# Kernel optimization log

Hardware: AMD Instinct MI355X
Metric: run time of the kernel (lower is better)

The kernel has to match this reference:

```python
import jax, jax.numpy as jnp
import numpy as np

SEQ_LEN, USER_LEN = 20, 256
INPUT_SIZE = 100000
NUM_CENTROIDS = 64
CAND = 1024
HIDDEN_DIM = 128
TOPK = 10
RHO = 0.02


def setup_inputs() -> dict:
    key = jax.random.key(0)
    ks = jax.random.split(key, 20)
    s = 0.1  # modest weight scale
    return {
        "x": jax.random.randint(ks[0], (SEQ_LEN, USER_LEN), 0, INPUT_SIZE),
        "t_slot": jax.random.randint(ks[1], (SEQ_LEN, USER_LEN), 0, 168),
        "vecs_use": jax.random.normal(ks[2], (INPUT_SIZE, 20), jnp.float32),
        "x_embedding_network": jax.random.normal(ks[3], (INPUT_SIZE, HIDDEN_DIM), jnp.float32),
        "I_array": jax.random.randint(ks[4], (INPUT_SIZE,), 0, NUM_CENTROIDS),
        "cand": jax.random.randint(ks[5], (NUM_CENTROIDS, CAND), 0, INPUT_SIZE),
        "time_embeddings": jax.random.normal(ks[6], (4, 20), jnp.float32),
        "W_seq1": jax.random.normal(ks[7], (100, 40), jnp.float32) * s,
        "b_seq1": jnp.zeros((40,), jnp.float32),
        "W_seq2": jax.random.normal(ks[8], (40, 20), jnp.float32) * s,
        "b_seq2": jnp.zeros((20,), jnp.float32),
        "W_to1": jax.random.normal(ks[9], (40, 40), jnp.float32) * s,
        "b_to1": jnp.zeros((40,), jnp.float32),
        "W_to2": jax.random.normal(ks[10], (40, 20), jnp.float32) * s,
        "b_to2": jnp.zeros((20,), jnp.float32),
        "W_ti1": jax.random.normal(ks[11], (40, 40), jnp.float32) * s,
        "b_ti1": jnp.zeros((40,), jnp.float32),
        "W_ti2": jax.random.normal(ks[12], (40, 20), jnp.float32) * s,
        "b_ti2": jnp.zeros((20,), jnp.float32),
    }


def _map_hour_to_segment(t):
    h = t % 24
    return jnp.where((h >= 22) | (h < 6), 0, jnp.where(h < 14, 1, 2))


def reference(x, t_slot, vecs_use, x_embedding_network, I_array, cand,
              time_embeddings, W_seq1, b_seq1, W_seq2, b_seq2,
              W_to1, b_to1, W_to2, b_to2, W_ti1, b_ti1, W_ti2, b_ti2):
    seq_len, user_len = x.shape
    x_view = x.reshape(-1)                                  # [N]
    x_emb = vecs_use[x_view].reshape(seq_len, user_len, 20)  # [S,U,20]

    # time-transfer (outgoing): concat(loc_emb, time_emb[segment]) -> MLP
    seg = _map_hour_to_segment(t_slot.reshape(-1))
    xc = jnp.concatenate([x_emb.reshape(-1, 20), time_embeddings[seg]], axis=-1)
    xi_out = jax.nn.relu(xc @ W_to1 + b_to1) @ W_to2 + b_to2  # [N,20]

    # candidate side: every location paired with fixed target segment 2
    seg2 = jnp.broadcast_to(time_embeddings[2], (vecs_use.shape[0], 20))
    vo = jnp.concatenate([vecs_use, seg2], axis=-1)
    vec_output = jax.nn.relu(vo @ W_ti1 + b_ti1) @ W_ti2 + b_ti2  # [V,20]

    # 5-step history (shift-with-edge-repeat) concat -> seq MLP
    def shift(k):
        return jnp.concatenate([x_emb[:k], x_emb[:seq_len - k]], axis=0)
    hist = jnp.concatenate(
        [shift(4), shift(3), shift(2), shift(1), x_emb], axis=-1).reshape(-1, 100)
    hist = jax.nn.relu(hist @ W_seq1 + b_seq1) @ W_seq2 + b_seq2  # [N,20]

    # per-token cluster routing + candidate distances
    a = 0.5 * (hist + xi_out)            # [N,20]
    c_idx = I_array[x_view]              # [N] cluster of each token's location
    cand_tok = cand[c_idx]               # [N,C] candidate loc ids
    Vg = vec_output[cand_tok]            # [N,C,20]
    d2 = (jnp.sum(a * a, -1)[:, None] + jnp.sum(Vg * Vg, -1)
          - 2.0 * jnp.einsum('nd,ncd->nc', a, Vg))
    dist = jnp.sqrt(jnp.maximum(d2, 1e-12))
    score = jnp.exp(-RHO * dist)         # [N,C]

    values, idx = jax.lax.top_k(score, TOPK)                 # [N,K]
    neigh_ids = jnp.take_along_axis(cand_tok, idx, axis=1)   # [N,K]
    emb_neigh = x_embedding_network[neigh_ids]               # [N,K,H]
    self_emb = x_embedding_network[x_view][:, None, :]       # [N,1,H]
    emb_all = jnp.concatenate([emb_neigh, self_emb], axis=1)  # [N,K+1,H]
    vals = jnp.concatenate(
        [values, jnp.ones((values.shape[0], 1), values.dtype)], axis=-1)
    w = jax.nn.softmax(vals, axis=-1)                        # [N,K+1]
    return jnp.sum(emb_all * w[..., None], axis=1)           # [N,H]
```

## Files before the change

### kernel.cpp

```cpp
#include <hip/hip_runtime.h>
#include <hip/hip_bf16.h>

#define SEQ_LEN   20
#define USER_LEN  256
#define NTOK      (SEQ_LEN * USER_LEN)
#define NC        64
#define CAND_N    1024
#define HID       128
#define TOPK      10
#define RHO_C     0.02f

#define CAND_BLKS 256
#define TO_BLKS   (NTOK / 256)
#define SEQ_BLKS  (NTOK / 256)
#define MAXB      (NTOK / 8 + NC)

__global__ __launch_bounds__(256) void k_pre(
    const int* __restrict__ x, const int* __restrict__ t_slot,
    const float* __restrict__ vecs, const float* __restrict__ temb,
    const int* __restrict__ I_array, const int* __restrict__ cand,
    const float* __restrict__ Ws1, const float* __restrict__ bs1,
    const float* __restrict__ Ws2, const float* __restrict__ bs2,
    const float* __restrict__ Wt1, const float* __restrict__ bt1,
    const float* __restrict__ Wt2, const float* __restrict__ bt2,
    const float* __restrict__ Wc1, const float* __restrict__ bc1,
    const float* __restrict__ Wc2, const float* __restrict__ bc2,
    float* __restrict__ tab, float* __restrict__ aX, float* __restrict__ aH,
    int* __restrict__ bucket, int* __restrict__ blkInfo) {
  __shared__ float sWS[4800];
  int tid = threadIdx.x;

  if (blockIdx.x < CAND_BLKS) {
    {
      float4* dst = (float4*)sWS;
      const float4* s1 = (const float4*)Wc1;
      for (int i = tid; i < 400; i += 256) dst[i] = s1[i];
      const float4* s2 = (const float4*)Wc2;
      for (int i = tid; i < 200; i += 256) dst[400 + i] = s2[i];
    }
    __syncthreads();
    const float* sW1 = sWS;
    const float* sW2 = sWS + 1600;

    int g = blockIdx.x * 256 + tid;
    int v = cand[g];
    const float4* vp = (const float4*)(vecs + (size_t)v * 20);
    const float4* tp = (const float4*)(temb + 40);

    float o[20];
    #pragma unroll
    for (int k = 0; k < 20; k++) o[k] = bc2[k];

    #pragma unroll 1
    for (int cc = 0; cc < 5; cc++) {
      float hc[8];
      #pragma unroll
      for (int jj = 0; jj < 8; jj++) hc[jj] = bc1[cc * 8 + jj];
      #pragma unroll
      for (int q = 0; q < 5; q++) {
        float4 e = tp[q];
        #pragma unroll
        for (int r = 0; r < 4; r++) {
          float xi = (&e.x)[r];
          const float* wr = &sW1[(20 + 4 * q + r) * 40 + cc * 8];
          float4 w0 = *(const float4*)(wr);
          float4 w1 = *(const float4*)(wr + 4);
          hc[0] = fmaf(xi, w0.x, hc[0]); hc[1] = fmaf(xi, w0.y, hc[1]);
          hc[2] = fmaf(xi, w0.z, hc[2]); hc[3] = fmaf(xi, w0.w, hc[3]);
          hc[4] = fmaf(xi, w1.x, hc[4]); hc[5] = fmaf(xi, w1.y, hc[5]);
          hc[6] = fmaf(xi, w1.z, hc[6]); hc[7] = fmaf(xi, w1.w, hc[7]);
        }
      }
      #pragma unroll
      for (int q = 0; q < 5; q++) {
        float4 e = vp[q];
        #pragma unroll
        for (int r = 0; r < 4; r++) {
          float xi = (&e.x)[r];
          const float* wr = &sW1[(4 * q + r) * 40 + cc * 8];
          float4 w0 = *(const float4*)(wr);
          float4 w1 = *(const float4*)(wr + 4);
          hc[0] = fmaf(xi, w0.x, hc[0]); hc[1] = fmaf(xi, w0.y, hc[1]);
          hc[2] = fmaf(xi, w0.z, hc[2]); hc[3] = fmaf(xi, w0.w, hc[3]);
          hc[4] = fmaf(xi, w1.x, hc[4]); hc[5] = fmaf(xi, w1.y, hc[5]);
          hc[6] = fmaf(xi, w1.z, hc[6]); hc[7] = fmaf(xi, w1.w, hc[7]);
        }
      }
      #pragma unroll
      for (int jj = 0; jj < 8; jj++) {
        float hv = fmaxf(hc[jj], 0.f);
        const float* wr = &sW2[(cc * 8 + jj) * 20];
        #pragma unroll
        for (int kq = 0; kq < 5; kq++) {
          float4 w = *(const float4*)(wr + 4 * kq);
          o[kq * 4 + 0] = fmaf(hv, w.x, o[kq * 4 + 0]);
          o[kq * 4 + 1] = fmaf(hv, w.y, o[kq * 4 + 1]);
          o[kq * 4 + 2] = fmaf(hv, w.z, o[kq * 4 + 2]);
          o[kq * 4 + 3] = fmaf(hv, w.w, o[kq * 4 + 3]);
        }
      }
    }
    int c = g >> 10, j = g & 1023;
    float* op = tab + (size_t)c * (21 * CAND_N) + j;
    float nrm = 0.f;
    #pragma unroll
    for (int k = 0; k < 20; k++) {
      op[k * CAND_N] = o[k];
      nrm = fmaf(o[k], o[k], nrm);
    }
    op[20 * CAND_N] = nrm;

  } else if (blockIdx.x < CAND_BLKS + TO_BLKS) {
    {
      float4* dst = (float4*)sWS;
      const float4* s1 = (const float4*)Wt1;
      for (int i = tid; i < 400; i += 256) dst[i] = s1[i];
      const float4* s2 = (const float4*)Wt2;
      for (int i = tid; i < 200; i += 256) dst[400 + i] = s2[i];
    }
    __syncthreads();
    const float* sW1 = sWS;
    const float* sW2 = sWS + 1600;

    int n = (blockIdx.x - CAND_BLKS) * 256 + tid;
    int xv = x[n];
    int ts = t_slot[n];
    int h24 = ts % 24;
    int seg = (h24 >= 22 || h24 < 6) ? 0 : (h24 < 14 ? 1 : 2);
    const float4* ep = (const float4*)(vecs + (size_t)xv * 20);
    const float4* tp = (const float4*)(temb + seg * 20);

    float o[20];
    #pragma unroll
    for (int k = 0; k < 20; k++) o[k] = bt2[k];

    #pragma unroll 1
    for (int cc = 0; cc < 5; cc++) {
      float hc[8];
      #pragma unroll
      for (int jj = 0; jj < 8; jj++) hc[jj] = bt1[cc * 8 + jj];
      #pragma unroll
      for (int q = 0; q < 5; q++) {
        float4 e = ep[q];
        #pragma unroll
        for (int r = 0; r < 4; r++) {
          float xi = (&e.x)[r];
          const float* wr = &sW1[(4 * q + r) * 40 + cc * 8];
          float4 w0 = *(const float4*)(wr);
          float4 w1 = *(const float4*)(wr + 4);
          hc[0] = fmaf(xi, w0.x, hc[0]); hc[1] = fmaf(xi, w0.y, hc[1]);
          hc[2] = fmaf(xi, w0.z, hc[2]); hc[3] = fmaf(xi, w0.w, hc[3]);
          hc[4] = fmaf(xi, w1.x, hc[4]); hc[5] = fmaf(xi, w1.y, hc[5]);
          hc[6] = fmaf(xi, w1.z, hc[6]); hc[7] = fmaf(xi, w1.w, hc[7]);
        }
      }
      #pragma unroll
      for (int q = 0; q < 5; q++) {
        float4 e = tp[q];
        #pragma unroll
        for (int r = 0; r < 4; r++) {
          float xi = (&e.x)[r];
          const float* wr = &sW1[(20 + 4 * q + r) * 40 + cc * 8];
          float4 w0 = *(const float4*)(wr);
          float4 w1 = *(const float4*)(wr + 4);
          hc[0] = fmaf(xi, w0.x, hc[0]); hc[1] = fmaf(xi, w0.y, hc[1]);
          hc[2] = fmaf(xi, w0.z, hc[2]); hc[3] = fmaf(xi, w0.w, hc[3]);
          hc[4] = fmaf(xi, w1.x, hc[4]); hc[5] = fmaf(xi, w1.y, hc[5]);
          hc[6] = fmaf(xi, w1.z, hc[6]); hc[7] = fmaf(xi, w1.w, hc[7]);
        }
      }
      #pragma unroll
      for (int jj = 0; jj < 8; jj++) {
        float hv = fmaxf(hc[jj], 0.f);
        const float* wr = &sW2[(cc * 8 + jj) * 20];
        #pragma unroll
        for (int kq = 0; kq < 5; kq++) {
          float4 w = *(const float4*)(wr + 4 * kq);
          o[kq * 4 + 0] = fmaf(hv, w.x, o[kq * 4 + 0]);
          o[kq * 4 + 1] = fmaf(hv, w.y, o[kq * 4 + 1]);
          o[kq * 4 + 2] = fmaf(hv, w.z, o[kq * 4 + 2]);
          o[kq * 4 + 3] = fmaf(hv, w.w, o[kq * 4 + 3]);
        }
      }
    }
    #pragma unroll
    for (int k = 0; k < 20; k++) aX[n * 20 + k] = o[k];

  } else if (blockIdx.x < CAND_BLKS + TO_BLKS + SEQ_BLKS) {
    {
      float4* dst = (float4*)sWS;
      const float4* s1 = (const float4*)Ws1;
      for (int i = tid; i < 1000; i += 256) dst[i] = s1[i];
      const float4* s2 = (const float4*)Ws2;
      for (int i = tid; i < 200; i += 256) dst[1000 + i] = s2[i];
    }
    __syncthreads();
    const float* sW1 = sWS;
    const float* sW2 = sWS + 4000;

    int n = (blockIdx.x - CAND_BLKS - TO_BLKS) * 256 + tid;
    int s = n >> 8, u = n & 255;
    int xv2[5];
    #pragma unroll
    for (int b = 0; b < 5; b++) {
      int sh = 4 - b;
      int row = (s >= sh) ? s - sh : s;
      xv2[b] = x[row * USER_LEN + u];
    }

    float o[20];
    #pragma unroll
    for (int k = 0; k < 20; k++) o[k] = bs2[k];

    #pragma unroll 1
    for (int cc = 0; cc < 5; cc++) {
      float hc[8];
      #pragma unroll
      for (int jj = 0; jj < 8; jj++) hc[jj] = bs1[cc * 8 + jj];
      #pragma unroll 1
      for (int b = 0; b < 5; b++) {
        const float4* p = (const float4*)(vecs + (size_t)xv2[b] * 20);
        #pragma unroll
        for (int q = 0; q < 5; q++) {
          float4 e = p[q];
          #pragma unroll
          for (int r = 0; r < 4; r++) {
            float xi = (&e.x)[r];
            const float* wr = &sW1[(b * 20 + 4 * q + r) * 40 + cc * 8];
            float4 w0 = *(const float4*)(wr);
            float4 w1 = *(const float4*)(wr + 4);
            hc[0] = fmaf(xi, w0.x, hc[0]); hc[1] = fmaf(xi, w0.y, hc[1]);
            hc[2] = fmaf(xi, w0.z, hc[2]); hc[3] = fmaf(xi, w0.w, hc[3]);
            hc[4] = fmaf(xi, w1.x, hc[4]); hc[5] = fmaf(xi, w1.y, hc[5]);
            hc[6] = fmaf(xi, w1.z, hc[6]); hc[7] = fmaf(xi, w1.w, hc[7]);
          }
        }
      }
      #pragma unroll
      for (int jj = 0; jj < 8; jj++) {
        float hv = fmaxf(hc[jj], 0.f);
        const float* wr = &sW2[(cc * 8 + jj) * 20];
        #pragma unroll
        for (int kq = 0; kq < 5; kq++) {
          float4 w = *(const float4*)(wr + 4 * kq);
          o[kq * 4 + 0] = fmaf(hv, w.x, o[kq * 4 + 0]);
          o[kq * 4 + 1] = fmaf(hv, w.y, o[kq * 4 + 1]);
          o[kq * 4 + 2] = fmaf(hv, w.z, o[kq * 4 + 2]);
          o[kq * 4 + 3] = fmaf(hv, w.w, o[kq * 4 + 3]);
        }
      }
    }
    #pragma unroll
    for (int k = 0; k < 20; k++) aH[n * 20 + k] = o[k];

  } else {
    int* lc = (int*)sWS;
    int* lcur = lc + NC;
    if (tid < NC) lc[tid] = 0;
    for (int b = tid; b < MAXB; b += 256) blkInfo[b] = -1;
    __syncthreads();
    for (int n = tid; n < NTOK; n += 256)
      atomicAdd(&lc[I_array[x[n]]], 1);
    __syncthreads();

    int v = 0, myStart = 0, nb = 0, blkStart = 0;
    if (tid < 64) {
      v = lc[tid];
      int inc = v;
      #pragma unroll
      for (int d = 1; d < 64; d <<= 1) {
        int t2 = __shfl_up(inc, d);
        if (tid >= d) inc += t2;
      }
      myStart = inc - v;
      lcur[tid] = myStart;
      nb = (v + 7) >> 3;
      int nbs = nb;
      #pragma unroll
      for (int d = 1; d < 64; d <<= 1) {
        int t2 = __shfl_up(nbs, d);
        if (tid >= d) nbs += t2;
      }
      blkStart = nbs - nb;
    }
    __syncthreads();
    for (int n = tid; n < NTOK; n += 256) {
      int c = I_array[x[n]];
      int p = atomicAdd(&lcur[c], 1);
      bucket[p] = n;
    }
    if (tid < 64) {
      for (int k = 0; k < nb; k++) {
        int rem = v - 8 * k;
        int tc = rem < 8 ? rem : 8;
        blkInfo[blkStart + k] = (tid << 20) | (tc << 16) | (myStart + 8 * k);
      }
    }
  }
}

__global__ __launch_bounds__(256) void k_distsel(
    const int* __restrict__ blkInfo, const int* __restrict__ bucket,
    const float* __restrict__ tab, const float* __restrict__ aX,
    const float* __restrict__ aH, const int* __restrict__ x,
    const int* __restrict__ cand, const float* __restrict__ emb,
    float* __restrict__ out) {
  int info = blkInfo[blockIdx.x];
  if (info < 0) return;
  int start = info & 0xFFFF;
  int tcnt  = (info >> 16) & 0xF;
  int c     = info >> 20;

  __shared__ float sA[8][20];
  __shared__ float sN[8];
  __shared__ int   sTok[8];
  __shared__ float sD[8][CAND_N];

  int tid = threadIdx.x;
  if (tid < 8) sTok[tid] = (tid < tcnt) ? bucket[start + tid] : -1;
  if (tid < 160) {
    int tt = tid / 20, d = tid - tt * 20;
    if (tt < tcnt) {
      int n = bucket[start + tt];
      sA[tt][d] = 0.5f * (aH[n * 20 + d] + aX[n * 20 + d]);
    } else {
      sA[tt][d] = 0.f;
    }
  }
  __syncthreads();
  if (tid < 8) {
    float nrm = 0.f;
    #pragma unroll
    for (int d = 0; d < 20; d++) nrm = fmaf(sA[tid][d], sA[tid][d], nrm);
    sN[tid] = nrm;
  }
  __syncthreads();

  const float* T = tab + (size_t)c * (21 * CAND_N);
  int j4 = tid * 4;
  float4 acc[8];
  #pragma unroll
  for (int tt = 0; tt < 8; tt++) acc[tt] = make_float4(0.f, 0.f, 0.f, 0.f);
  #pragma unroll
  for (int dq = 0; dq < 5; dq++) {
    float4 t0 = *(const float4*)(T + (dq * 4 + 0) * CAND_N + j4);
    float4 t1 = *(const float4*)(T + (dq * 4 + 1) * CAND_N + j4);
    float4 t2 = *(const float4*)(T + (dq * 4 + 2) * CAND_N + j4);
    float4 t3 = *(const float4*)(T + (dq * 4 + 3) * CAND_N + j4);
    #pragma unroll
    for (int tt = 0; tt < 8; tt++) {
      float4 av = *(const float4*)(&sA[tt][dq * 4]);
      acc[tt].x = fmaf(av.x, t0.x, acc[tt].x);
      acc[tt].y = fmaf(av.x, t0.y, acc[tt].y);
      acc[tt].z = fmaf(av.x, t0.z, acc[tt].z);
      acc[tt].w = fmaf(av.x, t0.w, acc[tt].w);
      acc[tt].x = fmaf(av.y, t1.x, acc[tt].x);
      acc[tt].y = fmaf(av.y, t1.y, acc[tt].y);
      acc[tt].z = fmaf(av.y, t1.z, acc[tt].z);
      acc[tt].w = fmaf(av.y, t1.w, acc[tt].w);
      acc[tt].x = fmaf(av.z, t2.x, acc[tt].x);
      acc[tt].y = fmaf(av.z, t2.y, acc[tt].y);
      acc[tt].z = fmaf(av.z, t2.z, acc[tt].z);
      acc[tt].w = fmaf(av.z, t2.w, acc[tt].w);
      acc[tt].x = fmaf(av.w, t3.x, acc[tt].x);
      acc[tt].y = fmaf(av.w, t3.y, acc[tt].y);
      acc[tt].z = fmaf(av.w, t3.z, acc[tt].z);
      acc[tt].w = fmaf(av.w, t3.w, acc[tt].w);
    }
  }
  float4 cn4 = *(const float4*)(T + 20 * CAND_N + j4);
  #pragma unroll
  for (int tt = 0; tt < 8; tt++) {
    float4 d2;
    d2.x = sN[tt] + cn4.x - 2.f * acc[tt].x;
    d2.y = sN[tt] + cn4.y - 2.f * acc[tt].y;
    d2.z = sN[tt] + cn4.z - 2.f * acc[tt].z;
    d2.w = sN[tt] + cn4.w - 2.f * acc[tt].w;
    *(float4*)(&sD[tt][j4]) = d2;
  }
  __syncthreads();

  int lane = tid & 63, w = tid >> 6;
  #pragma unroll 1
  for (int pass = 0; pass < 2; pass++) {
    int tt = w + 4 * pass;
    if (tt >= tcnt) continue;
    int n = sTok[tt];
    int xv = x[n];

    float v[16];
    #pragma unroll
    for (int m = 0; m < 16; m++) v[m] = sD[tt][m * 64 + lane];

    float acc0 = 0.f, acc1 = 0.f, esum = 0.f;
    #pragma unroll 1
    for (int r = 0; r < TOPK; r++) {
      float bv = v[0];
      int bj = lane;
      #pragma unroll
      for (int m = 1; m < 16; m++) {
        int jm = (m << 6) | lane;
        if (v[m] < bv) { bv = v[m]; bj = jm; }
      }
      #pragma unroll
      for (int o = 1; o < 64; o <<= 1) {
        float ov = __shfl_xor(bv, o);
        int   oj = __shfl_xor(bj, o);
        if (ov < bv || (ov == bv && oj < bj)) { bv = ov; bj = oj; }
      }
      float dist = sqrtf(fmaxf(bv, 1e-12f));
      float e = expf(expf(-RHO_C * dist));
      int id = cand[c * CAND_N + bj];
      esum += e;
      acc0 = fmaf(e, emb[(size_t)id * HID + lane], acc0);
      acc1 = fmaf(e, emb[(size_t)id * HID + 64 + lane], acc1);
      #pragma unroll
      for (int m = 0; m < 16; m++) {
        int jm = (m << 6) | lane;
        if (jm == bj) v[m] = 3.0e38f;
      }
    }
    const float e1 = 2.71828182845904523536f;
    esum += e1;
    acc0 = fmaf(e1, emb[(size_t)xv * HID + lane], acc0);
    acc1 = fmaf(e1, emb[(size_t)xv * HID + 64 + lane], acc1);
    float inv = 1.0f / esum;
    out[(size_t)n * HID + lane] = acc0 * inv;
    out[(size_t)n * HID + 64 + lane] = acc1 * inv;
  }
}

extern "C" void kernel_launch(void* const* d_in, const int* in_sizes, int n_in,
                              void* d_out, int out_size, void* d_ws, size_t ws_size,
                              hipStream_t stream) {
  const int*   x      = (const int*)d_in[0];
  const int*   t_slot = (const int*)d_in[1];
  const float* vecs   = (const float*)d_in[2];
  const float* embn   = (const float*)d_in[3];
  const int*   I_arr  = (const int*)d_in[4];
  const int*   cand   = (const int*)d_in[5];
  const float* temb   = (const float*)d_in[6];
  const float* Ws1    = (const float*)d_in[7];
  const float* bs1    = (const float*)d_in[8];
  const float* Ws2    = (const float*)d_in[9];
  const float* bs2    = (const float*)d_in[10];
  const float* Wto1   = (const float*)d_in[11];
  const float* bto1   = (const float*)d_in[12];
  const float* Wto2   = (const float*)d_in[13];
  const float* bto2   = (const float*)d_in[14];
  const float* Wti1   = (const float*)d_in[15];
  const float* bti1   = (const float*)d_in[16];
  const float* Wti2   = (const float*)d_in[17];
  const float* bti2   = (const float*)d_in[18];

  float* tab    = (float*)d_ws;
  float* aX     = tab + NC * 21 * CAND_N;
  float* aH     = aX + NTOK * 20;
  int*   bucket = (int*)(aH + NTOK * 20);
  int*   blkInfo= bucket + NTOK;
  float* outp   = (float*)d_out;

  k_pre<<<CAND_BLKS + TO_BLKS + SEQ_BLKS + 1, 256, 0, stream>>>(
      x, t_slot, vecs, temb, I_arr, cand,
      Ws1, bs1, Ws2, bs2, Wto1, bto1, Wto2, bto2,
      Wti1, bti1, Wti2, bti2,
      tab, aX, aH, bucket, blkInfo);
  k_distsel<<<MAXB, 256, 0, stream>>>(blkInfo, bucket, tab, aX, aH,
                                      x, cand, embn, outp);
}
```

Measured before the change: 177.5 us.

## Precompute time-embedding MLP contributions per block and spread token MLPs over more blocks

The candidate and time-transfer MLP first layers now split out the time-embedding half: the time-embedding part plus bias is computed once per block (one segment for candidates, three for tokens) into shared memory and used as the hidden init. This removes 20 of 40 input FMAs per hidden unit per thread. The time-transfer and sequence MLP branches also use four times as many blocks with only 64 active threads each, to spread the latency-bound per-token work across more CUs. The cost is that each such block still loads its full weights into shared memory while three quarters of its threads sit idle.

```diff
diff --git a/kernel.cpp b/kernel.cpp
--- a/kernel.cpp
+++ b/kernel.cpp
@@ -11,8 +11,8 @@
 #define RHO_C     0.02f
 
 #define CAND_BLKS 256
-#define TO_BLKS   (NTOK / 256)
-#define SEQ_BLKS  (NTOK / 256)
+#define TO_BLKS   (NTOK / 64)
+#define SEQ_BLKS  (NTOK / 64)
 #define MAXB      (NTOK / 8 + NC)
 
 __global__ __launch_bounds__(256) void k_pre(
@@ -34,18 +34,25 @@
     {
       float4* dst = (float4*)sWS;
       const float4* s1 = (const float4*)Wc1;
-      for (int i = tid; i < 400; i += 256) dst[i] = s1[i];
+      for (int i = tid; i < 200; i += 256) dst[i] = s1[i];
       const float4* s2 = (const float4*)Wc2;
-      for (int i = tid; i < 200; i += 256) dst[400 + i] = s2[i];
+      for (int i = tid; i < 200; i += 256) dst[200 + i] = s2[i];
+    }
+    if (tid < 40) {
+      float acc = bc1[tid];
+      #pragma unroll 4
+      for (int i = 0; i < 20; i++)
+        acc = fmaf(temb[40 + i], Wc1[(20 + i) * 40 + tid], acc);
+      sWS[1600 + tid] = acc;
     }
     __syncthreads();
     const float* sW1 = sWS;
-    const float* sW2 = sWS + 1600;
+    const float* sW2 = sWS + 800;
+    const float* sHt = sWS + 1600;
 
     int g = blockIdx.x * 256 + tid;
     int v = cand[g];
     const float4* vp = (const float4*)(vecs + (size_t)v * 20);
-    const float4* tp = (const float4*)(temb + 40);
 
     float o[20];
     #pragma unroll
@@ -55,22 +62,7 @@
     for (int cc = 0; cc < 5; cc++) {
       float hc[8];
       #pragma unroll
-      for (int jj = 0; jj < 8; jj++) hc[jj] = bc1[cc * 8 + jj];
-      #pragma unroll
-      for (int q = 0; q < 5; q++) {
-        float4 e = tp[q];
-        #pragma unroll
-        for (int r = 0; r < 4; r++) {
-          float xi = (&e.x)[r];
-          const float* wr = &sW1[(20 + 4 * q + r) * 40 + cc * 8];
-          float4 w0 = *(const float4*)(wr);
-          float4 w1 = *(const float4*)(wr + 4);
-          hc[0] = fmaf(xi, w0.x, hc[0]); hc[1] = fmaf(xi, w0.y, hc[1]);
-          hc[2] = fmaf(xi, w0.z, hc[2]); hc[3] = fmaf(xi, w0.w, hc[3]);
-          hc[4] = fmaf(xi, w1.x, hc[4]); hc[5] = fmaf(xi, w1.y, hc[5]);
-          hc[6] = fmaf(xi, w1.z, hc[6]); hc[7] = fmaf(xi, w1.w, hc[7]);
-        }
-      }
+      for (int jj = 0; jj < 8; jj++) hc[jj] = sHt[cc * 8 + jj];
       #pragma unroll
       for (int q = 0; q < 5; q++) {
         float4 e = vp[q];
@@ -114,77 +106,73 @@
     {
       float4* dst = (float4*)sWS;
       const float4* s1 = (const float4*)Wt1;
-      for (int i = tid; i < 400; i += 256) dst[i] = s1[i];
+      for (int i = tid; i < 200; i += 256) dst[i] = s1[i];
       const float4* s2 = (const float4*)Wt2;
-      for (int i = tid; i < 200; i += 256) dst[400 + i] = s2[i];
+      for (int i = tid; i < 200; i += 256) dst[200 + i] = s2[i];
+    }
+    if (tid < 120) {
+      int sg = tid / 40, j = tid - sg * 40;
+      float acc = bt1[j];
+      #pragma unroll 4
+      for (int i = 0; i < 20; i++)
+        acc = fmaf(temb[sg * 20 + i], Wt1[(20 + i) * 40 + j], acc);
+      sWS[1600 + tid] = acc;
     }
     __syncthreads();
     const float* sW1 = sWS;
-    const float* sW2 = sWS + 1600;
-
-    int n = (blockIdx.x - CAND_BLKS) * 256 + tid;
-    int xv = x[n];
-    int ts = t_slot[n];
-    int h24 = ts % 24;
-    int seg = (h24 >= 22 || h24 < 6) ? 0 : (h24 < 14 ? 1 : 2);
-    const float4* ep = (const float4*)(vecs + (size_t)xv * 20);
-    const float4* tp = (const float4*)(temb + seg * 20);
-
-    float o[20];
-    #pragma unroll
-    for (int k = 0; k < 20; k++) o[k] = bt2[k];
-
-    #pragma unroll 1
-    for (int cc = 0; cc < 5; cc++) {
-      float hc[8];
-      #pragma unroll
-      for (int jj = 0; jj < 8; jj++) hc[jj] = bt1[cc * 8 + jj];
-      #pragma unroll
-      for (int q = 0; q < 5; q++) {
-        float4 e = ep[q];
-        #pragma unroll
-        for (int r = 0; r < 4; r++) {
-          float xi = (&e.x)[r];
-          const float* wr = &sW1[(4 * q + r) * 40 + cc * 8];
-          float4 w0 = *(const float4*)(wr);
-          float4 w1 = *(const float4*)(wr + 4);
-          hc[0] = fmaf(xi, w0.x, hc[0]); hc[1] = fmaf(xi, w0.y, hc[1]);
-          hc[2] = fmaf(xi, w0.z, hc[2]); hc[3] = fmaf(xi, w0.w, hc[3]);
-          hc[4] = fmaf(xi, w1.x, hc[4]); hc[5] = fmaf(xi, w1.y, hc[5]);
-          hc[6] = fmaf(xi, w1.z, hc[6]); hc[7] = fmaf(xi, w1.w, hc[7]);
-        }
-      }
-      #pragma unroll
-      for (int q = 0; q < 5; q++) {
-        float4 e = tp[q];
-        #pragma unroll
-        for (int r = 0; r < 4; r++) {
-          float xi = (&e.x)[r];
-          const float* wr = &sW1[(20 + 4 * q + r) * 40 + cc * 8];
-          float4 w0 = *(const float4*)(wr);
-          float4 w1 = *(const float4*)(wr + 4);
-          hc[0] = fmaf(xi, w0.x, hc[0]); hc[1] = fmaf(xi, w0.y, hc[1]);
-          hc[2] = fmaf(xi, w0.z, hc[2]); hc[3] = fmaf(xi, w0.w, hc[3]);
-          hc[4] = fmaf(xi, w1.x, hc[4]); hc[5] = fmaf(xi, w1.y, hc[5]);
-          hc[6] = fmaf(xi, w1.z, hc[6]); hc[7] = fmaf(xi, w1.w, hc[7]);
-        }
-      }
-      #pragma unroll
-      for (int jj = 0; jj < 8; jj++) {
-        float hv = fmaxf(hc[jj], 0.f);
-        const float* wr = &sW2[(cc * 8 + jj) * 20];
-        #pragma unroll
-        for (int kq = 0; kq < 5; kq++) {
-          float4 w = *(const float4*)(wr + 4 * kq);
-          o[kq * 4 + 0] = fmaf(hv, w.x, o[kq * 4 + 0]);
-          o[kq * 4 + 1] = fmaf(hv, w.y, o[kq * 4 + 1]);
-          o[kq * 4 + 2] = fmaf(hv, w.z, o[kq * 4 + 2]);
-          o[kq * 4 + 3] = fmaf(hv, w.w, o[kq * 4 + 3]);
-        }
-      }
-    }
-    #pragma unroll
-    for (int k = 0; k < 20; k++) aX[n * 20 + k] = o[k];
+    const float* sW2 = sWS + 800;
+    const float* sHt3 = sWS + 1600;
+
+    if (tid < 64) {
+      int n = (blockIdx.x - CAND_BLKS) * 64 + tid;
+      int xv = x[n];
+      int ts = t_slot[n];
+      int h24 = ts % 24;
+      int seg = (h24 >= 22 || h24 < 6) ? 0 : (h24 < 14 ? 1 : 2);
+      const float4* ep = (const float4*)(vecs + (size_t)xv * 20);
+      const float* ht = sHt3 + seg * 40;
+
+      float o[20];
+      #pragma unroll
+      for (int k = 0; k < 20; k++) o[k] = bt2[k];
+
+      #pragma unroll 1
+      for (int cc = 0; cc < 5; cc++) {
+        float hc[8];
+        #pragma unroll
+        for (int jj = 0; jj < 8; jj++) hc[jj] = ht[cc * 8 + jj];
+        #pragma unroll
+        for (int q = 0; q < 5; q++) {
+          float4 e = ep[q];
+          #pragma unroll
+          for (int r = 0; r < 4; r++) {
+            float xi = (&e.x)[r];
+            const float* wr = &sW1[(4 * q + r) * 40 + cc * 8];
+            float4 w0 = *(const float4*)(wr);
+            float4 w1 = *(const float4*)(wr + 4);
+            hc[0] = fmaf(xi, w0.x, hc[0]); hc[1] = fmaf(xi, w0.y, hc[1]);
+            hc[2] = fmaf(xi, w0.z, hc[2]); hc[3] = fmaf(xi, w0.w, hc[3]);
+            hc[4] = fmaf(xi, w1.x, hc[4]); hc[5] = fmaf(xi, w1.y, hc[5]);
+            hc[6] = fmaf(xi, w1.z, hc[6]); hc[7] = fmaf(xi, w1.w, hc[7]);
+          }
+        }
+        #pragma unroll
+        for (int jj = 0; jj < 8; jj++) {
+          float hv = fmaxf(hc[jj], 0.f);
+          const float* wr = &sW2[(cc * 8 + jj) * 20];
+          #pragma unroll
+          for (int kq = 0; kq < 5; kq++) {
+            float4 w = *(const float4*)(wr + 4 * kq);
+            o[kq * 4 + 0] = fmaf(hv, w.x, o[kq * 4 + 0]);
+            o[kq * 4 + 1] = fmaf(hv, w.y, o[kq * 4 + 1]);
+            o[kq * 4 + 2] = fmaf(hv, w.z, o[kq * 4 + 2]);
+            o[kq * 4 + 3] = fmaf(hv, w.w, o[kq * 4 + 3]);
+          }
+        }
+      }
+      #pragma unroll
+      for (int k = 0; k < 20; k++) aX[n * 20 + k] = o[k];
+    }
 
   } else if (blockIdx.x < CAND_BLKS + TO_BLKS + SEQ_BLKS) {
     {
@@ -198,60 +186,62 @@
     const float* sW1 = sWS;
     const float* sW2 = sWS + 4000;
 
-    int n = (blockIdx.x - CAND_BLKS - TO_BLKS) * 256 + tid;
-    int s = n >> 8, u = n & 255;
-    int xv2[5];
-    #pragma unroll
-    for (int b = 0; b < 5; b++) {
-      int sh = 4 - b;
-      int row = (s >= sh) ? s - sh : s;
-      xv2[b] = x[row * USER_LEN + u];
-    }
-
-    float o[20];
-    #pragma unroll
-    for (int k = 0; k < 20; k++) o[k] = bs2[k];
-
-    #pragma unroll 1
-    for (int cc = 0; cc < 5; cc++) {
-      float hc[8];
-      #pragma unroll
-      for (int jj = 0; jj < 8; jj++) hc[jj] = bs1[cc * 8 + jj];
+    if (tid < 64) {
+      int n = (blockIdx.x - CAND_BLKS - TO_BLKS) * 64 + tid;
+      int s = n >> 8, u = n & 255;
+      int xv2[5];
+      #pragma unroll
+      for (int b = 0; b < 5; b++) {
+        int sh = 4 - b;
+        int row = (s >= sh) ? s - sh : s;
+        xv2[b] = x[row * USER_LEN + u];
+      }
+
+      float o[20];
+      #pragma unroll
+      for (int k = 0; k < 20; k++) o[k] = bs2[k];
+
       #pragma unroll 1
-      for (int b = 0; b < 5; b++) {
-        const float4* p = (const float4*)(vecs + (size_t)xv2[b] * 20);
-        #pragma unroll
-        for (int q = 0; q < 5; q++) {
-          float4 e = p[q];
+      for (int cc = 0; cc < 5; cc++) {
+        float hc[8];
+        #pragma unroll
+        for (int jj = 0; jj < 8; jj++) hc[jj] = bs1[cc * 8 + jj];
+        #pragma unroll 1
+        for (int b = 0; b < 5; b++) {
+          const float4* p = (const float4*)(vecs + (size_t)xv2[b] * 20);
           #pragma unroll
-          for (int r = 0; r < 4; r++) {
-            float xi = (&e.x)[r];
-            const float* wr = &sW1[(b * 20 + 4 * q + r) * 40 + cc * 8];
-            float4 w0 = *(const float4*)(wr);
-            float4 w1 = *(const float4*)(wr + 4);
-            hc[0] = fmaf(xi, w0.x, hc[0]); hc[1] = fmaf(xi, w0.y, hc[1]);
-            hc[2] = fmaf(xi, w0.z, hc[2]); hc[3] = fmaf(xi, w0.w, hc[3]);
-            hc[4] = fmaf(xi, w1.x, hc[4]); hc[5] = fmaf(xi, w1.y, hc[5]);
-            hc[6] = fmaf(xi, w1.z, hc[6]); hc[7] = fmaf(xi, w1.w, hc[7]);
+          for (int q = 0; q < 5; q++) {
+            float4 e = p[q];
+            #pragma unroll
+            for (int r = 0; r < 4; r++) {
+              float xi = (&e.x)[r];
+              const float* wr = &sW1[(b * 20 + 4 * q + r) * 40 + cc * 8];
+              float4 w0 = *(const float4*)(wr);
+              float4 w1 = *(const float4*)(wr + 4);
+              hc[0] = fmaf(xi, w0.x, hc[0]); hc[1] = fmaf(xi, w0.y, hc[1]);
+              hc[2] = fmaf(xi, w0.z, hc[2]); hc[3] = fmaf(xi, w0.w, hc[3]);
+              hc[4] = fmaf(xi, w1.x, hc[4]); hc[5] = fmaf(xi, w1.y, hc[5]);
+              hc[6] = fmaf(xi, w1.z, hc[6]); hc[7] = fmaf(xi, w1.w, hc[7]);
+            }
           }
         }
-      }
-      #pragma unroll
-      for (int jj = 0; jj < 8; jj++) {
-        float hv = fmaxf(hc[jj], 0.f);
-        const float* wr = &sW2[(cc * 8 + jj) * 20];
-        #pragma unroll
-        for (int kq = 0; kq < 5; kq++) {
-          float4 w = *(const float4*)(wr + 4 * kq);
-          o[kq * 4 + 0] = fmaf(hv, w.x, o[kq * 4 + 0]);
-          o[kq * 4 + 1] = fmaf(hv, w.y, o[kq * 4 + 1]);
-          o[kq * 4 + 2] = fmaf(hv, w.z, o[kq * 4 + 2]);
-          o[kq * 4 + 3] = fmaf(hv, w.w, o[kq * 4 + 3]);
-        }
-      }
-    }
-    #pragma unroll
-    for (int k = 0; k < 20; k++) aH[n * 20 + k] = o[k];
+        #pragma unroll
+        for (int jj = 0; jj < 8; jj++) {
+          float hv = fmaxf(hc[jj], 0.f);
+          const float* wr = &sW2[(cc * 8 + jj) * 20];
+          #pragma unroll
+          for (int kq = 0; kq < 5; kq++) {
+            float4 w = *(const float4*)(wr + 4 * kq);
+            o[kq * 4 + 0] = fmaf(hv, w.x, o[kq * 4 + 0]);
+            o[kq * 4 + 1] = fmaf(hv, w.y, o[kq * 4 + 1]);
+            o[kq * 4 + 2] = fmaf(hv, w.z, o[kq * 4 + 2]);
+            o[kq * 4 + 3] = fmaf(hv, w.w, o[kq * 4 + 3]);
+          }
+        }
+      }
+      #pragma unroll
+      for (int k = 0; k < 20; k++) aH[n * 20 + k] = o[k];
+    }
 
   } else {
     int* lc = (int*)sWS;
```

New measurement: 178.5 us. About the same (+0.6%).
